# Kernel optimization log

Hardware: AMD Instinct MI355X
Metric: run time of the kernel (lower is better)

The kernel has to match this reference:

```python
import jax, jax.numpy as jnp
import numpy as np

B, NV, NH, D = 16, 1024, 1024, 1024
NEG = -1e30


def setup_inputs() -> dict:
    key = jax.random.key(0)
    ks = jax.random.split(key, 12)
    sc = 1.0 / np.sqrt(D)
    return {
        "v": jax.random.normal(ks[0], (B, NV, D), jnp.float32),
        "h": jax.random.normal(ks[1], (B, NH, D), jnp.float32),
        "z": jax.random.normal(ks[2], (B, NV, 2 * D), jnp.float32),
        "v_mask": jnp.ones((B, NV), jnp.int32),
        "h_mask": jnp.ones((B, NH), jnp.int32),
        # learned parameters (torch Linear convention: W [out,in])
        "Wv_w": jax.random.normal(ks[3], (D, D), jnp.float32) * sc,
        "Wv_b": jax.random.normal(ks[4], (D,), jnp.float32) * sc,
        "Wh_w": jax.random.normal(ks[5], (D, D), jnp.float32) * sc,
        "qv_w": jax.random.normal(ks[6], (D, D), jnp.float32) * sc,
        "qv_b": jax.random.normal(ks[7], (D,), jnp.float32) * sc,
        "kh_w": jax.random.normal(ks[8], (D, D), jnp.float32) * sc,
        "Wz_w": jax.random.normal(ks[9], (D, 2 * D), jnp.float32) * sc,
        "Wu_w": jax.random.normal(ks[10], (1, D), jnp.float32) * sc,
    }


def reference(v, h, z, v_mask, h_mask, Wv_w, Wv_b, Wh_w, qv_w, qv_b, kh_w, Wz_w, Wu_w):
    v_v = v @ Wv_w.T + Wv_b                    # [B,NV,D]
    h_h = h @ Wh_w.T                           # [B,NH,D]
    z_z = z @ Wz_w.T                           # [B,NV,D]
    query = v @ qv_w.T + qv_b                  # [B,NV,D]
    key = h @ kh_w.T                           # [B,NH,D]
    key = jnp.where(h_mask[:, :, None] == 0, NEG, key)
    att = jnp.einsum('bqd,bkd->bqk', query, key)       # [B,NV,NH]
    h_v = jnp.einsum('bqk,bkd->bqd', jax.nn.softmax(att, axis=-1), h_h)
    s = jax.nn.sigmoid(v_v + h_v + z_z)        # [B,NV,D]
    # W_u(s_i + s_j) == u_i + u_j since W_u is linear with no bias
    u = jnp.einsum('bnd,d->bn', s, Wu_w[0])    # [B,NV]
    f = u[:, :, None] + u[:, None, :]          # [B,NV,NV] pairwise scores
    f = jnp.where(v_mask[:, None, :] == 0, NEG, f)
    f = jnp.einsum('bij,bjd->bid', jax.nn.softmax(f, axis=-1), v)  # [B,NV,D]
    h_new = f
    z_new = jnp.concatenate((s, f), axis=-1)   # [B,NV,2D]
    return h_new, z_new
```

## Files before the change

### kernel.cpp

```cpp
#include <hip/hip_runtime.h>

#define BB 16
#define NV 1024
#define NH 1024
#define DD 1024

typedef _Float16 f16x8 __attribute__((ext_vector_type(8)));
typedef _Float16 f16x4 __attribute__((ext_vector_type(4)));
typedef float f32x4 __attribute__((ext_vector_type(4)));

__global__ __launch_bounds__(256) void cast_k(const float* __restrict__ in,
                                              _Float16* __restrict__ out, long n4) {
  long i = (long)blockIdx.x * 256 + threadIdx.x;
  long stride = (long)gridDim.x * 256;
  for (; i < n4; i += stride) {
    float4 x = ((const float4*)in)[i];
    f16x4 o;
    o[0] = (_Float16)x.x; o[1] = (_Float16)x.y;
    o[2] = (_Float16)x.z; o[3] = (_Float16)x.w;
    ((f16x4*)out)[i] = o;
  }
}

__global__ __launch_bounds__(256) void split_k(const float* __restrict__ in,
                                               _Float16* __restrict__ hi,
                                               _Float16* __restrict__ lo, long n4) {
  long i = (long)blockIdx.x * 256 + threadIdx.x;
  long stride = (long)gridDim.x * 256;
  for (; i < n4; i += stride) {
    float4 x = ((const float4*)in)[i];
    f16x4 h, l;
    h[0] = (_Float16)x.x; h[1] = (_Float16)x.y;
    h[2] = (_Float16)x.z; h[3] = (_Float16)x.w;
    l[0] = (_Float16)(x.x - (float)h[0]);
    l[1] = (_Float16)(x.y - (float)h[1]);
    l[2] = (_Float16)(x.z - (float)h[2]);
    l[3] = (_Float16)(x.w - (float)h[3]);
    ((f16x4*)hi)[i] = h;
    ((f16x4*)lo)[i] = l;
  }
}

__device__ inline void gl_lds16(const _Float16* g, _Float16* l) {
  __builtin_amdgcn_global_load_lds((__attribute__((address_space(1))) void*)g,
                                   (__attribute__((address_space(3))) void*)l,
                                   16, 0, 0);
}

__device__ inline void decode256(int flat, int NB, int& bm, int& bn, int& bz) {
  int xcd = flat & 7, j = flat >> 3;
  if (NB == 1) {
    bz = 0;
    bm = xcd * 8 + (j >> 2);
    bn = j & 3;
  } else {
    bz = xcd * 2 + (j >> 4);
    int r = j & 15;
    bm = r >> 2;
    bn = r & 3;
  }
}


template <typename CT>
__global__ __launch_bounds__(512) void gemm256_nt_k(
    const _Float16* __restrict__ A, const _Float16* __restrict__ B,
    CT* __restrict__ C, const float* __restrict__ bias,
    int K, int NB, long sA, long sB, long sC) {
  __shared__ _Float16 lds[65536];
  const int tid = threadIdx.x;
  const int w = tid >> 6, l = tid & 63;
  int bm, bn, bz;
  decode256(blockIdx.x, NB, bm, bn, bz);
  const _Float16* Ab = A + (long)bz * sA;
  const _Float16* Bb = B + (long)bz * sB;
  CT* Cb = C + (long)bz * sC;

  const int srow = w * 16 + (l >> 2);
  const int sslot = (l & 3) ^ ((l >> 3) & 3);
  const _Float16* gA = Ab + (long)(bm * 256 + srow) * K + sslot * 8;
  const _Float16* gB = Bb + (long)(bn * 256 + srow) * K + sslot * 8;
  const long rs128 = (long)128 * K;
  const int T = K >> 5;

  const int fr = l & 15, fq = l >> 4;
  const int sw = (fr >> 1) & 3;
  const int wm = w >> 2, wn = w & 3;
  const int aoff = (wm * 128 + fr) * 32 + (fq ^ sw) * 8;
  const int boff = (wn * 64 + fr) * 32 + (fq ^ sw) * 8;

  f32x4 acc[8][4] = {};

  auto stageA = [&](int st) {
    _Float16* dA = lds + (st & 3) * 16384 + w * 512;
    const _Float16* pA = gA + st * 32;
    gl_lds16(pA, dA);
    gl_lds16(pA + rs128, dA + 4096);
  };
  auto stageB = [&](int st) {
    _Float16* dB = lds + (st & 3) * 16384 + 8192 + w * 512;
    const _Float16* pB = gB + st * 32;
    gl_lds16(pB, dB);
    gl_lds16(pB + rs128, dB + 4096);
  };

  stageA(0); stageB(0); stageA(1); stageB(1); stageA(2); stageB(2);
  asm volatile("s_waitcnt vmcnt(8)" ::: "memory");
  __builtin_amdgcn_s_barrier();
  __builtin_amdgcn_sched_barrier(0);

  for (int t = 0; t < T; ++t) {
    const _Float16* bufA = lds + (t & 3) * 16384;
    const _Float16* bufB = bufA + 8192;
    f16x8 af[8], bf[4];
#pragma unroll
    for (int n = 0; n < 4; ++n) bf[n] = *(const f16x8*)&bufB[boff + n * 512];
#pragma unroll
    for (int m = 0; m < 2; ++m) af[m] = *(const f16x8*)&bufA[aoff + m * 512];
    __builtin_amdgcn_s_setprio(1);
#pragma unroll
    for (int m = 0; m < 2; ++m)
#pragma unroll
      for (int n = 0; n < 4; ++n)
        acc[m][n] = __builtin_amdgcn_mfma_f32_16x16x32_f16(af[m], bf[n], acc[m][n], 0, 0, 0);
    __builtin_amdgcn_s_setprio(0);
    __builtin_amdgcn_sched_barrier(0);
#pragma unroll
    for (int m = 2; m < 4; ++m) af[m] = *(const f16x8*)&bufA[aoff + m * 512];
    __builtin_amdgcn_s_setprio(1);
#pragma unroll
    for (int m = 2; m < 4; ++m)
#pragma unroll
      for (int n = 0; n < 4; ++n)
        acc[m][n] = __builtin_amdgcn_mfma_f32_16x16x32_f16(af[m], bf[n], acc[m][n], 0, 0, 0);
    __builtin_amdgcn_s_setprio(0);
    __builtin_amdgcn_s_barrier();
    __builtin_amdgcn_sched_barrier(0);
#pragma unroll
    for (int m = 4; m < 6; ++m) af[m] = *(const f16x8*)&bufA[aoff + m * 512];
    if (t + 3 < T) stageA(t + 3);
    __builtin_amdgcn_s_setprio(1);
#pragma unroll
    for (int m = 4; m < 6; ++m)
#pragma unroll
      for (int n = 0; n < 4; ++n)
        acc[m][n] = __builtin_amdgcn_mfma_f32_16x16x32_f16(af[m], bf[n], acc[m][n], 0, 0, 0);
    __builtin_amdgcn_s_setprio(0);
    __builtin_amdgcn_sched_barrier(0);
#pragma unroll
    for (int m = 6; m < 8; ++m) af[m] = *(const f16x8*)&bufA[aoff + m * 512];
    if (t + 3 < T) stageB(t + 3);
    __builtin_amdgcn_s_setprio(1);
#pragma unroll
    for (int m = 6; m < 8; ++m)
#pragma unroll
      for (int n = 0; n < 4; ++n)
        acc[m][n] = __builtin_amdgcn_mfma_f32_16x16x32_f16(af[m], bf[n], acc[m][n], 0, 0, 0);
    __builtin_amdgcn_s_setprio(0);
    if (t + 1 < T) {
      const int hi = (t + 3 < T) ? t + 3 : T - 1;
      const int cnt = 4 * (hi - (t + 1));
      if (cnt >= 8)      asm volatile("s_waitcnt vmcnt(8)" ::: "memory");
      else if (cnt == 4) asm volatile("s_waitcnt vmcnt(4)" ::: "memory");
      else               asm volatile("s_waitcnt vmcnt(0)" ::: "memory");
      __builtin_amdgcn_s_barrier();
      __builtin_amdgcn_sched_barrier(0);
    }
  }

#pragma unroll
  for (int m = 0; m < 8; ++m) {
    const int grow = bm * 256 + wm * 128 + m * 16 + fq * 4;
#pragma unroll
    for (int n = 0; n < 4; ++n) {
      const int gcol = bn * 256 + wn * 64 + n * 16 + fr;
      const float bv = bias ? bias[gcol] : 0.0f;
#pragma unroll
      for (int e = 0; e < 4; ++e)
        Cb[(long)(grow + e) * 1024 + gcol] = (CT)(acc[m][n][e] + bv);
    }
  }
}

template <bool SPLIT_OUT>
__global__ __launch_bounds__(512) void gemm3_256_k(
    const _Float16* __restrict__ Ahi, const _Float16* __restrict__ Alo,
    const _Float16* __restrict__ Bhi, const _Float16* __restrict__ Blo,
    float* __restrict__ Cf, _Float16* __restrict__ Chi, _Float16* __restrict__ Clo,
    const float* __restrict__ bias, const int* __restrict__ mask,
    int K, int NB, long sA, long sB, long sC) {
  __shared__ _Float16 lds[65536];
  const int tid = threadIdx.x;
  const int w = tid >> 6, l = tid & 63;
  int bm, bn, bz;
  decode256(blockIdx.x, NB, bm, bn, bz);

  const int srow = w * 16 + (l >> 2);
  const int sslot = (l & 3) ^ ((l >> 3) & 3);
  const long abase = (long)(bm * 256 + srow) * K + sslot * 8 + (long)bz * sA;
  const long bbase = (long)(bn * 256 + srow) * K + sslot * 8 + (long)bz * sB;
  const _Float16* gAh = Ahi + abase;
  const _Float16* gAl = Alo + abase;
  const _Float16* gBh = Bhi + bbase;
  const _Float16* gBl = Blo + bbase;
  const long rs128 = (long)128 * K;
  const int T = K >> 5;

  const int fr = l & 15, fq = l >> 4;
  const int sw = (fr >> 1) & 3;
  const int wm = w >> 2, wn = w & 3;
  const int aoff = (wm * 128 + fr) * 32 + (fq ^ sw) * 8;
  const int boff = (wn * 64 + fr) * 32 + (fq ^ sw) * 8;

  f32x4 acc[8][4] = {};

  auto stageA3 = [&](int st) {
    _Float16* d = lds + (st & 1) * 32768 + w * 512;
    const int ko = st * 32;
    gl_lds16(gAh + ko, d);
    gl_lds16(gAh + ko + rs128, d + 4096);
    gl_lds16(gAl + ko, d + 8192);
    gl_lds16(gAl + ko + rs128, d + 12288);
  };
  auto stageB3 = [&](int st) {
    _Float16* d = lds + (st & 1) * 32768 + w * 512;
    const int ko = st * 32;
    gl_lds16(gBh + ko, d + 16384);
    gl_lds16(gBh + ko + rs128, d + 20480);
    gl_lds16(gBl + ko, d + 24576);
    gl_lds16(gBl + ko + rs128, d + 28672);
  };

  stageA3(0); stageB3(0); stageA3(1); stageB3(1);
  asm volatile("s_waitcnt vmcnt(8)" ::: "memory");
  __builtin_amdgcn_s_barrier();
  __builtin_amdgcn_sched_barrier(0);

  for (int t = 0; t < T; ++t) {
    const _Float16* bA = lds + (t & 1) * 32768;
    const _Float16* bB = bA + 16384;
    f16x8 ah[8], al[8], bh[4], bl[4];
#pragma unroll
    for (int n = 0; n < 4; ++n) {
      bh[n] = *(const f16x8*)&bB[boff + n * 512];
      bl[n] = *(const f16x8*)&bB[8192 + boff + n * 512];
    }
#pragma unroll
    for (int m = 0; m < 4; ++m) {
      ah[m] = *(const f16x8*)&bA[aoff + m * 512];
      al[m] = *(const f16x8*)&bA[8192 + aoff + m * 512];
    }
    __builtin_amdgcn_s_setprio(1);
#pragma unroll
    for (int m = 0; m < 2; ++m)
#pragma unroll
      for (int n = 0; n < 4; ++n) {
        acc[m][n] = __builtin_amdgcn_mfma_f32_16x16x32_f16(ah[m], bh[n], acc[m][n], 0, 0, 0);
        acc[m][n] = __builtin_amdgcn_mfma_f32_16x16x32_f16(al[m], bh[n], acc[m][n], 0, 0, 0);
        acc[m][n] = __builtin_amdgcn_mfma_f32_16x16x32_f16(ah[m], bl[n], acc[m][n], 0, 0, 0);
      }
    __builtin_amdgcn_s_setprio(0);
    __builtin_amdgcn_sched_barrier(0);
#pragma unroll
    for (int m = 4; m < 8; ++m) {
      ah[m] = *(const f16x8*)&bA[aoff + m * 512];
      al[m] = *(const f16x8*)&bA[8192 + aoff + m * 512];
    }
    __builtin_amdgcn_s_setprio(1);
#pragma unroll
    for (int m = 2; m < 4; ++m)
#pragma unroll
      for (int n = 0; n < 4; ++n) {
        acc[m][n] = __builtin_amdgcn_mfma_f32_16x16x32_f16(ah[m], bh[n], acc[m][n], 0, 0, 0);
        acc[m][n] = __builtin_amdgcn_mfma_f32_16x16x32_f16(al[m], bh[n], acc[m][n], 0, 0, 0);
        acc[m][n] = __builtin_amdgcn_mfma_f32_16x16x32_f16(ah[m], bl[n], acc[m][n], 0, 0, 0);
      }
    __builtin_amdgcn_s_setprio(0);
    asm volatile("s_waitcnt lgkmcnt(0)" ::: "memory");
    __builtin_amdgcn_s_barrier();
    __builtin_amdgcn_sched_barrier(0);
    if (t + 2 < T) stageA3(t + 2);
    __builtin_amdgcn_s_setprio(1);
#pragma unroll
    for (int m = 4; m < 6; ++m)
#pragma unroll
      for (int n = 0; n < 4; ++n) {
        acc[m][n] = __builtin_amdgcn_mfma_f32_16x16x32_f16(ah[m], bh[n], acc[m][n], 0, 0, 0);
        acc[m][n] = __builtin_amdgcn_mfma_f32_16x16x32_f16(al[m], bh[n], acc[m][n], 0, 0, 0);
        acc[m][n] = __builtin_amdgcn_mfma_f32_16x16x32_f16(ah[m], bl[n], acc[m][n], 0, 0, 0);
      }
    __builtin_amdgcn_s_setprio(0);
    __builtin_amdgcn_sched_barrier(0);
    if (t + 2 < T) stageB3(t + 2);
    __builtin_amdgcn_s_setprio(1);
#pragma unroll
    for (int m = 6; m < 8; ++m)
#pragma unroll
      for (int n = 0; n < 4; ++n) {
        acc[m][n] = __builtin_amdgcn_mfma_f32_16x16x32_f16(ah[m], bh[n], acc[m][n], 0, 0, 0);
        acc[m][n] = __builtin_amdgcn_mfma_f32_16x16x32_f16(al[m], bh[n], acc[m][n], 0, 0, 0);
        acc[m][n] = __builtin_amdgcn_mfma_f32_16x16x32_f16(ah[m], bl[n], acc[m][n], 0, 0, 0);
      }
    __builtin_amdgcn_s_setprio(0);
    if (t + 1 < T) {
      if (t + 2 < T) asm volatile("s_waitcnt vmcnt(8)" ::: "memory");
      else           asm volatile("s_waitcnt vmcnt(0)" ::: "memory");
      __builtin_amdgcn_s_barrier();
      __builtin_amdgcn_sched_barrier(0);
    }
  }

#pragma unroll
  for (int m = 0; m < 8; ++m) {
    const int grow = bm * 256 + wm * 128 + m * 16 + fq * 4;
#pragma unroll
    for (int n = 0; n < 4; ++n) {
      const int gcol = bn * 256 + wn * 64 + n * 16 + fr;
      const float bv = bias ? bias[gcol] : 0.0f;
#pragma unroll
      for (int e = 0; e < 4; ++e) {
        float val = acc[m][n][e] + bv;
        if (mask && mask[grow + e] == 0) val = -30000.0f;
        const long idx = (long)(grow + e) * 1024 + gcol + (long)bz * sC;
        if (SPLIT_OUT) {
          _Float16 hi = (_Float16)val;
          Chi[idx] = hi;
          Clo[idx] = (_Float16)(val - (float)hi);
        } else {
          Cf[idx] = val;
        }
      }
    }
  }
}

__device__ inline float wave_max(float v) {
#pragma unroll
  for (int o = 32; o > 0; o >>= 1) v = fmaxf(v, __shfl_xor(v, o, 64));
  return v;
}
__device__ inline float wave_sum(float v) {
#pragma unroll
  for (int o = 32; o > 0; o >>= 1) v += __shfl_xor(v, o, 64);
  return v;
}

__global__ __launch_bounds__(256) void softmax_rows_k(const float* __restrict__ att,
                                                      _Float16* __restrict__ P) {
  __shared__ float red[4];
  long row = blockIdx.x;
  int t = threadIdx.x, w = t >> 6;
  float4 x = ((const float4*)(att + row * 1024))[t];
  float m = fmaxf(fmaxf(x.x, x.y), fmaxf(x.z, x.w));
  m = wave_max(m);
  if ((t & 63) == 0) red[w] = m;
  __syncthreads();
  m = fmaxf(fmaxf(red[0], red[1]), fmaxf(red[2], red[3]));
  float e0 = expf(x.x - m), e1 = expf(x.y - m), e2 = expf(x.z - m), e3 = expf(x.w - m);
  float s = wave_sum(e0 + e1 + e2 + e3);
  __syncthreads();
  if ((t & 63) == 0) red[w] = s;
  __syncthreads();
  float inv = 1.0f / (red[0] + red[1] + red[2] + red[3]);
  f16x4 o;
  o[0] = (_Float16)(e0 * inv); o[1] = (_Float16)(e1 * inv);
  o[2] = (_Float16)(e2 * inv); o[3] = (_Float16)(e3 * inv);
  ((f16x4*)(P + row * 1024))[t] = o;
}

__global__ __launch_bounds__(256) void s_u_k(const _Float16* __restrict__ Vv,
                                             const float* __restrict__ Hv,
                                             const _Float16* __restrict__ Zz,
                                             const float* __restrict__ Wu,
                                             float* __restrict__ zout,
                                             float* __restrict__ u) {
  __shared__ float red[4];
  long row = blockIdx.x;
  int t = threadIdx.x, w = t >> 6;
  f16x4 a = ((const f16x4*)(Vv + row * 1024))[t];
  float4 b = ((const float4*)(Hv + row * 1024))[t];
  f16x4 c = ((const f16x4*)(Zz + row * 1024))[t];
  float4 wu = ((const float4*)Wu)[t];
  float4 sv;
  sv.x = 1.0f / (1.0f + expf(-((float)a[0] + b.x + (float)c[0])));
  sv.y = 1.0f / (1.0f + expf(-((float)a[1] + b.y + (float)c[1])));
  sv.z = 1.0f / (1.0f + expf(-((float)a[2] + b.z + (float)c[2])));
  sv.w = 1.0f / (1.0f + expf(-((float)a[3] + b.w + (float)c[3])));
  ((float4*)(zout + row * 2048))[t] = sv;
  float part = sv.x * wu.x + sv.y * wu.y + sv.z * wu.z + sv.w * wu.w;
  part = wave_sum(part);
  if ((t & 63) == 0) red[w] = part;
  __syncthreads();
  if (t == 0) u[row] = red[0] + red[1] + red[2] + red[3];
}

__global__ __launch_bounds__(256) void u_softmax_k(const float* __restrict__ u,
                                                   const int* __restrict__ vmask,
                                                   float* __restrict__ p) {
  __shared__ float red[4];
  int b = blockIdx.x, t = threadIdx.x, w = t >> 6;
  float4 uv = ((const float4*)(u + b * 1024))[t];
  int4 mv = ((const int4*)(vmask + b * 1024))[t];
  float l0 = mv.x ? uv.x : -1e30f;
  float l1 = mv.y ? uv.y : -1e30f;
  float l2 = mv.z ? uv.z : -1e30f;
  float l3 = mv.w ? uv.w : -1e30f;
  float m = wave_max(fmaxf(fmaxf(l0, l1), fmaxf(l2, l3)));
  if ((t & 63) == 0) red[w] = m;
  __syncthreads();
  m = fmaxf(fmaxf(red[0], red[1]), fmaxf(red[2], red[3]));
  float e0 = expf(l0 - m), e1 = expf(l1 - m), e2 = expf(l2 - m), e3 = expf(l3 - m);
  float s = wave_sum(e0 + e1 + e2 + e3);
  __syncthreads();
  if ((t & 63) == 0) red[w] = s;
  __syncthreads();
  float inv = 1.0f / (red[0] + red[1] + red[2] + red[3]);
  float4 o = make_float4(e0 * inv, e1 * inv, e2 * inv, e3 * inv);
  ((float4*)(p + b * 1024))[t] = o;
}

__global__ __launch_bounds__(256) void f_part_k(const float* __restrict__ p,
                                               const float* __restrict__ v,
                                               float* __restrict__ f) {
  int d = blockIdx.x * 256 + threadIdx.x;
  int b = blockIdx.y;
  int jc = blockIdx.z;
  const float* vb = v + ((long)b * NV + jc * 128) * DD + d;
  const float* pb = p + b * NV + jc * 128;
  float acc = 0.0f;
#pragma unroll 4
  for (int j = 0; j < 128; ++j) acc = fmaf(pb[j], vb[(long)j * DD], acc);
  atomicAdd(&f[b * DD + d], acc);
}

__global__ __launch_bounds__(256) void bcast_k(const float* __restrict__ f,
                                               float* __restrict__ hout,
                                               float* __restrict__ zout) {
  long idx = (long)blockIdx.x * 256 + threadIdx.x;
  int d4 = (int)(idx & 255);
  long bn = idx >> 8;
  int b = (int)(bn >> 10);
  float4 val = ((const float4*)f)[(b << 8) + d4];
  ((float4*)hout)[idx] = val;
  ((float4*)zout)[bn * 512 + 256 + d4] = val;
}

extern "C" void kernel_launch(void* const* d_in, const int* in_sizes, int n_in,
                              void* d_out, int out_size, void* d_ws, size_t ws_size,
                              hipStream_t stream) {
  const float* v = (const float*)d_in[0];
  const float* h = (const float*)d_in[1];
  const float* z = (const float*)d_in[2];
  const int* v_mask = (const int*)d_in[3];
  const int* h_mask = (const int*)d_in[4];
  const float* Wv_w = (const float*)d_in[5];
  const float* Wv_b = (const float*)d_in[6];
  const float* Wh_w = (const float*)d_in[7];
  const float* qv_w = (const float*)d_in[8];
  const float* qv_b = (const float*)d_in[9];
  const float* kh_w = (const float*)d_in[10];
  const float* Wz_w = (const float*)d_in[11];
  const float* Wu_w = (const float*)d_in[12];

  float* h_new = (float*)d_out;
  float* z_new = (float*)d_out + (long)BB * NV * DD;

  const size_t MB = 1u << 20;
  char* W = (char*)d_ws;
  _Float16* vhi  = (_Float16*)(W + 0 * MB);
  _Float16* vlo  = (_Float16*)(W + 32 * MB);
  _Float16* P16  = (_Float16*)(W + 32 * MB);
  _Float16* hhi  = (_Float16*)(W + 64 * MB);
  _Float16* hlo  = (_Float16*)(W + 96 * MB);
  _Float16* Hht16 = (_Float16*)(W + 96 * MB);
  _Float16* z16  = (_Float16*)(W + 128 * MB);
  _Float16* qvhi = (_Float16*)(W + 192 * MB);
  _Float16* qvlo = (_Float16*)(W + 194 * MB);
  _Float16* khhi = (_Float16*)(W + 196 * MB);
  _Float16* khlo = (_Float16*)(W + 198 * MB);
  _Float16* Wv16 = (_Float16*)(W + 200 * MB);
  _Float16* Wh16 = (_Float16*)(W + 202 * MB);
  _Float16* Wz16 = (_Float16*)(W + 204 * MB);
  _Float16* Qhi  = (_Float16*)(W + 208 * MB);
  _Float16* Vv16 = (_Float16*)(W + 208 * MB);
  _Float16* Qlo  = (_Float16*)(W + 240 * MB);
  _Float16* Zz16 = (_Float16*)(W + 240 * MB);
  _Float16* Khi  = (_Float16*)(W + 272 * MB);
  _Float16* Klo  = (_Float16*)(W + 304 * MB);
  float*    Hv32 = (float*)(W + 272 * MB);
  float*    att32 = (float*)(W + 336 * MB);
  float*    u_buf = (float*)(W + 400 * MB);
  float*    p_buf = (float*)(W + 400 * MB + 65536);
  float*    f_buf = (float*)(W + 400 * MB + 2 * 65536);

  const long nVD = (long)BB * NV * DD;
  const long s1M = (long)NV * DD;

  auto cast = [&](const float* src, _Float16* dst, long n) {
    long n4 = n / 4;
    cast_k<<<(int)((n4 + 255) / 256), 256, 0, stream>>>(src, dst, n4);
  };
  auto split = [&](const float* src, _Float16* hi, _Float16* lo, long n) {
    long n4 = n / 4;
    split_k<<<(int)((n4 + 255) / 256), 256, 0, stream>>>(src, hi, lo, n4);
  };

  split(v, vhi, vlo, nVD);
  split(h, hhi, hlo, nVD);
  cast(z, z16, nVD * 2);
  split(qv_w, qvhi, qvlo, (long)DD * DD);
  split(kh_w, khhi, khlo, (long)DD * DD);
  cast(Wv_w, Wv16, (long)DD * DD);
  cast(Wh_w, Wh16, (long)DD * DD);
  cast(Wz_w, Wz16, (long)DD * 2 * DD);

  gemm3_256_k<true><<<256, 512, 0, stream>>>(vhi, vlo, qvhi, qvlo,
      nullptr, Qhi, Qlo, qv_b, nullptr, DD, 1, 0, 0, 0);
  gemm3_256_k<true><<<256, 512, 0, stream>>>(hhi, hlo, khhi, khlo,
      nullptr, Khi, Klo, nullptr, h_mask, DD, 1, 0, 0, 0);
  gemm3_256_k<false><<<256, 512, 0, stream>>>(Qhi, Qlo, Khi, Klo,
      att32, nullptr, nullptr, nullptr, nullptr, DD, BB, s1M, s1M, s1M);
  softmax_rows_k<<<BB * NV, 256, 0, stream>>>(att32, P16);
  gemm256_nt_k<_Float16><<<256, 512, 0, stream>>>(Wh16, hhi, Hht16, nullptr, DD, BB, 0, s1M, s1M);
  gemm256_nt_k<_Float16><<<256, 512, 0, stream>>>(vhi, Wv16, Vv16, Wv_b, DD, 1, 0, 0, 0);
  gemm256_nt_k<_Float16><<<256, 512, 0, stream>>>(z16, Wz16, Zz16, nullptr, 2 * DD, 1, 0, 0, 0);
  gemm256_nt_k<float><<<256, 512, 0, stream>>>(P16, Hht16, Hv32, nullptr, NH, BB, s1M, s1M, s1M);
  s_u_k<<<BB * NV, 256, 0, stream>>>(Vv16, Hv32, Zz16, Wu_w, z_new, u_buf);
  u_softmax_k<<<BB, 256, 0, stream>>>(u_buf, v_mask, p_buf);
  hipMemsetAsync(f_buf, 0, (long)BB * DD * 4, stream);
  f_part_k<<<dim3(4, BB, 8), 256, 0, stream>>>(p_buf, v, f_buf);
  bcast_k<<<(int)(nVD / 4 / 256), 256, 0, stream>>>(f_buf, h_new, z_new);
}
```

Measured before the change: 1.023 ms.

## Restructure GEMM main loops into barrier-synchronized ping-pong phases with split staging

Both GEMM kernels' inner loops are reorganized so that each phase issues LDS fragment reads, hits a workgroup barrier and an lgkmcnt(0) wait, then runs a larger block of MFMAs. This follows a ping-pong pattern intended to keep wave groups alternating between memory and compute. In the three-term split-precision kernel, the hi*hi, lo*hi and hi*lo products are now grouped per phase instead of interleaved, which lets fewer fragments stay live at once. Global-to-LDS staging is also split into three roughly equal chunks spread across the phases. The extra barriers add synchronization cost, and changing the vmcnt accounting (6 loads per stage) while keeping the wait at vmcnt(8) could mistime waits.

```diff
diff --git a/kernel.cpp b/kernel.cpp
--- a/kernel.cpp
+++ b/kernel.cpp
@@ -47,6 +47,10 @@
                                    16, 0, 0);
 }
 
+#define SB0() __builtin_amdgcn_sched_barrier(0)
+#define BAR() __builtin_amdgcn_s_barrier()
+#define LGKM0() asm volatile("s_waitcnt lgkmcnt(0)" ::: "memory")
+
 __device__ inline void decode256(int flat, int NB, int& bm, int& bn, int& bz) {
   int xcd = flat & 7, j = flat >> 3;
   if (NB == 1) {
@@ -106,8 +110,7 @@
 
   stageA(0); stageB(0); stageA(1); stageB(1); stageA(2); stageB(2);
   asm volatile("s_waitcnt vmcnt(8)" ::: "memory");
-  __builtin_amdgcn_s_barrier();
-  __builtin_amdgcn_sched_barrier(0);
+  BAR(); SB0();
 
   for (int t = 0; t < T; ++t) {
     const _Float16* bufA = lds + (t & 3) * 16384;
@@ -116,43 +119,26 @@
 #pragma unroll
     for (int n = 0; n < 4; ++n) bf[n] = *(const f16x8*)&bufB[boff + n * 512];
 #pragma unroll
-    for (int m = 0; m < 2; ++m) af[m] = *(const f16x8*)&bufA[aoff + m * 512];
-    __builtin_amdgcn_s_setprio(1);
-#pragma unroll
-    for (int m = 0; m < 2; ++m)
+    for (int m = 0; m < 4; ++m) af[m] = *(const f16x8*)&bufA[aoff + m * 512];
+    if (t + 3 < T) stageA(t + 3);
+    BAR();
+    LGKM0(); SB0();
+    __builtin_amdgcn_s_setprio(1);
+#pragma unroll
+    for (int m = 0; m < 4; ++m)
 #pragma unroll
       for (int n = 0; n < 4; ++n)
         acc[m][n] = __builtin_amdgcn_mfma_f32_16x16x32_f16(af[m], bf[n], acc[m][n], 0, 0, 0);
     __builtin_amdgcn_s_setprio(0);
-    __builtin_amdgcn_sched_barrier(0);
-#pragma unroll
-    for (int m = 2; m < 4; ++m) af[m] = *(const f16x8*)&bufA[aoff + m * 512];
-    __builtin_amdgcn_s_setprio(1);
-#pragma unroll
-    for (int m = 2; m < 4; ++m)
-#pragma unroll
-      for (int n = 0; n < 4; ++n)
-        acc[m][n] = __builtin_amdgcn_mfma_f32_16x16x32_f16(af[m], bf[n], acc[m][n], 0, 0, 0);
-    __builtin_amdgcn_s_setprio(0);
-    __builtin_amdgcn_s_barrier();
-    __builtin_amdgcn_sched_barrier(0);
-#pragma unroll
-    for (int m = 4; m < 6; ++m) af[m] = *(const f16x8*)&bufA[aoff + m * 512];
-    if (t + 3 < T) stageA(t + 3);
-    __builtin_amdgcn_s_setprio(1);
-#pragma unroll
-    for (int m = 4; m < 6; ++m)
-#pragma unroll
-      for (int n = 0; n < 4; ++n)
-        acc[m][n] = __builtin_amdgcn_mfma_f32_16x16x32_f16(af[m], bf[n], acc[m][n], 0, 0, 0);
-    __builtin_amdgcn_s_setprio(0);
-    __builtin_amdgcn_sched_barrier(0);
-#pragma unroll
-    for (int m = 6; m < 8; ++m) af[m] = *(const f16x8*)&bufA[aoff + m * 512];
+    SB0();
+#pragma unroll
+    for (int m = 4; m < 8; ++m) af[m] = *(const f16x8*)&bufA[aoff + m * 512];
     if (t + 3 < T) stageB(t + 3);
-    __builtin_amdgcn_s_setprio(1);
-#pragma unroll
-    for (int m = 6; m < 8; ++m)
+    BAR();
+    LGKM0(); SB0();
+    __builtin_amdgcn_s_setprio(1);
+#pragma unroll
+    for (int m = 4; m < 8; ++m)
 #pragma unroll
       for (int n = 0; n < 4; ++n)
         acc[m][n] = __builtin_amdgcn_mfma_f32_16x16x32_f16(af[m], bf[n], acc[m][n], 0, 0, 0);
@@ -163,8 +149,7 @@
       if (cnt >= 8)      asm volatile("s_waitcnt vmcnt(8)" ::: "memory");
       else if (cnt == 4) asm volatile("s_waitcnt vmcnt(4)" ::: "memory");
       else               asm volatile("s_waitcnt vmcnt(0)" ::: "memory");
-      __builtin_amdgcn_s_barrier();
-      __builtin_amdgcn_sched_barrier(0);
+      BAR(); SB0();
     }
   }
 
@@ -214,99 +199,108 @@
 
   f32x4 acc[8][4] = {};
 
-  auto stageA3 = [&](int st) {
+  auto stage0 = [&](int st) {
     _Float16* d = lds + (st & 1) * 32768 + w * 512;
     const int ko = st * 32;
     gl_lds16(gAh + ko, d);
     gl_lds16(gAh + ko + rs128, d + 4096);
     gl_lds16(gAl + ko, d + 8192);
-    gl_lds16(gAl + ko + rs128, d + 12288);
-  };
-  auto stageB3 = [&](int st) {
+  };
+  auto stage1 = [&](int st) {
     _Float16* d = lds + (st & 1) * 32768 + w * 512;
     const int ko = st * 32;
+    gl_lds16(gAl + ko + rs128, d + 12288);
     gl_lds16(gBh + ko, d + 16384);
     gl_lds16(gBh + ko + rs128, d + 20480);
+  };
+  auto stage2 = [&](int st) {
+    _Float16* d = lds + (st & 1) * 32768 + w * 512;
+    const int ko = st * 32;
     gl_lds16(gBl + ko, d + 24576);
     gl_lds16(gBl + ko + rs128, d + 28672);
   };
 
-  stageA3(0); stageB3(0); stageA3(1); stageB3(1);
+  stage0(0); stage1(0); stage2(0); stage0(1); stage1(1); stage2(1);
   asm volatile("s_waitcnt vmcnt(8)" ::: "memory");
-  __builtin_amdgcn_s_barrier();
-  __builtin_amdgcn_sched_barrier(0);
+  BAR(); SB0();
 
   for (int t = 0; t < T; ++t) {
     const _Float16* bA = lds + (t & 1) * 32768;
     const _Float16* bB = bA + 16384;
     f16x8 ah[8], al[8], bh[4], bl[4];
 #pragma unroll
-    for (int n = 0; n < 4; ++n) {
-      bh[n] = *(const f16x8*)&bB[boff + n * 512];
-      bl[n] = *(const f16x8*)&bB[8192 + boff + n * 512];
-    }
-#pragma unroll
-    for (int m = 0; m < 4; ++m) {
-      ah[m] = *(const f16x8*)&bA[aoff + m * 512];
-      al[m] = *(const f16x8*)&bA[8192 + aoff + m * 512];
-    }
-    __builtin_amdgcn_s_setprio(1);
-#pragma unroll
-    for (int m = 0; m < 2; ++m)
-#pragma unroll
-      for (int n = 0; n < 4; ++n) {
+    for (int m = 0; m < 4; ++m) ah[m] = *(const f16x8*)&bA[aoff + m * 512];
+#pragma unroll
+    for (int n = 0; n < 4; ++n) bh[n] = *(const f16x8*)&bB[boff + n * 512];
+    BAR();
+    LGKM0(); SB0();
+    __builtin_amdgcn_s_setprio(1);
+#pragma unroll
+    for (int m = 0; m < 4; ++m)
+#pragma unroll
+      for (int n = 0; n < 4; ++n)
         acc[m][n] = __builtin_amdgcn_mfma_f32_16x16x32_f16(ah[m], bh[n], acc[m][n], 0, 0, 0);
+    __builtin_amdgcn_s_setprio(0);
+    SB0();
+#pragma unroll
+    for (int m = 4; m < 8; ++m) ah[m] = *(const f16x8*)&bA[aoff + m * 512];
+#pragma unroll
+    for (int m = 0; m < 4; ++m) al[m] = *(const f16x8*)&bA[8192 + aoff + m * 512];
+    BAR();
+    LGKM0(); SB0();
+    __builtin_amdgcn_s_setprio(1);
+#pragma unroll
+    for (int m = 4; m < 8; ++m)
+#pragma unroll
+      for (int n = 0; n < 4; ++n)
+        acc[m][n] = __builtin_amdgcn_mfma_f32_16x16x32_f16(ah[m], bh[n], acc[m][n], 0, 0, 0);
+    __builtin_amdgcn_s_setprio(0);
+    SB0();
+#pragma unroll
+    for (int m = 4; m < 8; ++m) al[m] = *(const f16x8*)&bA[8192 + aoff + m * 512];
+#pragma unroll
+    for (int n = 0; n < 4; ++n) bl[n] = *(const f16x8*)&bB[8192 + boff + n * 512];
+    BAR();
+    LGKM0(); SB0();
+    __builtin_amdgcn_s_setprio(1);
+#pragma unroll
+    for (int m = 0; m < 4; ++m)
+#pragma unroll
+      for (int n = 0; n < 4; ++n)
         acc[m][n] = __builtin_amdgcn_mfma_f32_16x16x32_f16(al[m], bh[n], acc[m][n], 0, 0, 0);
+    __builtin_amdgcn_s_setprio(0);
+    SB0();
+    BAR(); SB0();
+    if (t + 2 < T) stage0(t + 2);
+    __builtin_amdgcn_s_setprio(1);
+#pragma unroll
+    for (int m = 4; m < 8; ++m)
+#pragma unroll
+      for (int n = 0; n < 4; ++n)
+        acc[m][n] = __builtin_amdgcn_mfma_f32_16x16x32_f16(al[m], bh[n], acc[m][n], 0, 0, 0);
+    __builtin_amdgcn_s_setprio(0);
+    SB0();
+    if (t + 2 < T) stage1(t + 2);
+    __builtin_amdgcn_s_setprio(1);
+#pragma unroll
+    for (int m = 0; m < 4; ++m)
+#pragma unroll
+      for (int n = 0; n < 4; ++n)
         acc[m][n] = __builtin_amdgcn_mfma_f32_16x16x32_f16(ah[m], bl[n], acc[m][n], 0, 0, 0);
-      }
-    __builtin_amdgcn_s_setprio(0);
-    __builtin_amdgcn_sched_barrier(0);
-#pragma unroll
-    for (int m = 4; m < 8; ++m) {
-      ah[m] = *(const f16x8*)&bA[aoff + m * 512];
-      al[m] = *(const f16x8*)&bA[8192 + aoff + m * 512];
-    }
-    __builtin_amdgcn_s_setprio(1);
-#pragma unroll
-    for (int m = 2; m < 4; ++m)
-#pragma unroll
-      for (int n = 0; n < 4; ++n) {
-        acc[m][n] = __builtin_amdgcn_mfma_f32_16x16x32_f16(ah[m], bh[n], acc[m][n], 0, 0, 0);
-        acc[m][n] = __builtin_amdgcn_mfma_f32_16x16x32_f16(al[m], bh[n], acc[m][n], 0, 0, 0);
+    __builtin_amdgcn_s_setprio(0);
+    SB0();
+    if (t + 2 < T) stage2(t + 2);
+    __builtin_amdgcn_s_setprio(1);
+#pragma unroll
+    for (int m = 4; m < 8; ++m)
+#pragma unroll
+      for (int n = 0; n < 4; ++n)
         acc[m][n] = __builtin_amdgcn_mfma_f32_16x16x32_f16(ah[m], bl[n], acc[m][n], 0, 0, 0);
-      }
-    __builtin_amdgcn_s_setprio(0);
-    asm volatile("s_waitcnt lgkmcnt(0)" ::: "memory");
-    __builtin_amdgcn_s_barrier();
-    __builtin_amdgcn_sched_barrier(0);
-    if (t + 2 < T) stageA3(t + 2);
-    __builtin_amdgcn_s_setprio(1);
-#pragma unroll
-    for (int m = 4; m < 6; ++m)
-#pragma unroll
-      for (int n = 0; n < 4; ++n) {
-        acc[m][n] = __builtin_amdgcn_mfma_f32_16x16x32_f16(ah[m], bh[n], acc[m][n], 0, 0, 0);
-        acc[m][n] = __builtin_amdgcn_mfma_f32_16x16x32_f16(al[m], bh[n], acc[m][n], 0, 0, 0);
-        acc[m][n] = __builtin_amdgcn_mfma_f32_16x16x32_f16(ah[m], bl[n], acc[m][n], 0, 0, 0);
-      }
-    __builtin_amdgcn_s_setprio(0);
-    __builtin_amdgcn_sched_barrier(0);
-    if (t + 2 < T) stageB3(t + 2);
-    __builtin_amdgcn_s_setprio(1);
-#pragma unroll
-    for (int m = 6; m < 8; ++m)
-#pragma unroll
-      for (int n = 0; n < 4; ++n) {
-        acc[m][n] = __builtin_amdgcn_mfma_f32_16x16x32_f16(ah[m], bh[n], acc[m][n], 0, 0, 0);
-        acc[m][n] = __builtin_amdgcn_mfma_f32_16x16x32_f16(al[m], bh[n], acc[m][n], 0, 0, 0);
-        acc[m][n] = __builtin_amdgcn_mfma_f32_16x16x32_f16(ah[m], bl[n], acc[m][n], 0, 0, 0);
-      }
     __builtin_amdgcn_s_setprio(0);
     if (t + 1 < T) {
       if (t + 2 < T) asm volatile("s_waitcnt vmcnt(8)" ::: "memory");
       else           asm volatile("s_waitcnt vmcnt(0)" ::: "memory");
-      __builtin_amdgcn_s_barrier();
-      __builtin_amdgcn_sched_barrier(0);
+      BAR(); SB0();
     }
   }
 
```

Result: slower. 1.239 ms (+21.1%).
